# Optimization experiments

Measured on AMD Instinct MI355X. Metric: run time of the kernel, lower is better.

Reference implementation:

```python
import jax, jax.numpy as jnp
import numpy as np

B, K, C, NCLS = 256, 32, 2048, 20
EPS = 1e-4
MARGIN = 150.0
TRIP_MARGIN = 0.8
T = 0.07


def setup_inputs() -> dict:
    key = jax.random.key(0)
    ks = jax.random.split(key, 8)
    video_scores = jax.random.uniform(ks[0], (B, NCLS), jnp.float32, EPS, 1.0 - EPS)
    label = (jax.random.uniform(ks[1], (B, NCLS)) < 0.15).astype(jnp.float32)
    # guarantee every video has at least one positive class (avoids div-by-zero in label norm)
    fix = jax.nn.one_hot(jax.random.randint(ks[2], (B,), 0, NCLS), NCLS, dtype=jnp.float32)
    label = jnp.where((label.sum(axis=1, keepdims=True) > 0), label, fix)
    PA = jax.random.normal(ks[3], (B, K, C), jnp.float32)
    PB = jax.random.normal(ks[4], (B, K, C), jnp.float32)
    NA = jax.random.normal(ks[5], (B, K, C), jnp.float32)
    NB = jax.random.normal(ks[6], (B, K, C), jnp.float32)
    return {"video_scores": video_scores, "label": label, "PA": PA, "PB": PB, "NA": NA, "NB": NB}


def _nce(q, k, neg):
    # q,k: [B,C]; neg: [B,K,C] -> permuted to [B,C,K], normalized over C
    q = q / jnp.linalg.norm(q, axis=1, keepdims=True)
    k = k / jnp.linalg.norm(k, axis=1, keepdims=True)
    negp = jnp.transpose(neg, (0, 2, 1))  # [B,C,K]
    negp = negp / jnp.linalg.norm(negp, axis=1, keepdims=True)
    l_pos = jnp.einsum('nc,nc->n', q, k)[:, None]        # [B,1]
    l_neg = jnp.einsum('nc,nck->nk', q, negp)            # [B,K]
    logits = jnp.concatenate([l_pos, l_neg], axis=1) / T
    # CE with target class 0
    return -jax.nn.log_softmax(logits, axis=1)[:, 0].mean()


def _triplet(label, PA):
    n = label.shape[0]
    act = PA.mean(axis=2)  # [B,K] -- original averages over channels per snippet
    an = act / jnp.linalg.norm(act, axis=1, keepdims=True)
    D = 1.0 - an @ an.T    # [B,B] pairwise cosine distance
    idxs = jnp.arange(n)

    def per_class(m):  # m: bool [B] membership of this class
        cnt = m.sum()
        # anchor = last element of the Python set iteration = max member index
        anchor = jnp.max(jnp.where(m, idxs, -1))
        row = D[anchor]
        others = idxs != anchor
        max_d = jnp.maximum(0.0, jnp.max(jnp.where(m & others, row, -jnp.inf)))
        min_d = jnp.minimum(jnp.max(row), jnp.min(jnp.where(~m, row, jnp.inf)))
        contrib = jnp.maximum(max_d - min_d + TRIP_MARGIN, 0.0)
        return jnp.where(cnt > 1, contrib, 0.0)

    masks = (label == 1).T  # [NCLS, B]
    return jax.vmap(per_class)(masks).sum()


def reference(video_scores, label, PA, PB, NA, NB):
    # Action (BCE) loss with row-normalized labels
    lbl = label / label.sum(axis=1, keepdims=True)
    p = video_scores
    loss_cls = -(lbl * jnp.log(p) + (1.0 - lbl) * jnp.log(1.0 - p)).mean()

    # SniCo NCE
    loss_snico = _nce(NA.mean(axis=1), PA.mean(axis=1), PB) + _nce(NB.mean(axis=1), PB.mean(axis=1), PA)

    # Abs (uncertainty-margin) loss
    la = jnp.maximum(MARGIN - jnp.linalg.norm(PA.mean(axis=1), axis=1), 0.0)
    lb = jnp.linalg.norm(PB.mean(axis=1), axis=1)
    loss_abs = jnp.mean((la + lb) ** 2)

    # Triplet loss (vectorized version of the serial mining)
    loss_triplet = _triplet(label, PA)

    loss_total = loss_cls + 0.01 * loss_snico + 0.0005 * loss_abs + 0.005 * loss_triplet
    return (loss_total, loss_cls, loss_snico, loss_abs, loss_triplet)
```

## Files before the change

### kernel.cpp

```cpp
#include <hip/hip_runtime.h>
#include <math.h>

#define BATCH 256
#define KSNIP 32
#define CH    2048
#define CH4   512
#define NCLSS 20

#define OFF_MNA 0
#define OFF_MNB 524288
#define OFF_PK  1048576
#define PKN 8192
#define OFF_SC  1089536

__device__ __forceinline__ float dot4(float4 a, float4 b) {
    return a.x*b.x + a.y*b.y + a.z*b.z + a.w*b.w;
}
__device__ __forceinline__ float sum4(float4 a) { return a.x + a.y + a.z + a.w; }
__device__ __forceinline__ float4 add4(float4 a, float4 b) {
    return make_float4(a.x+b.x, a.y+b.y, a.z+b.z, a.w+b.w);
}

__global__ __launch_bounds__(512) void meanNK_kernel(
    const float* __restrict__ NAp, const float* __restrict__ NBp,
    float* __restrict__ ws)
{
    const int t   = blockIdx.x >> 8;
    const int b   = blockIdx.x & 255;
    const int tid = threadIdx.x;
    const int w   = tid >> 6;
    const int l   = tid & 63;

    const float4* src = (const float4*)((t ? NBp : NAp) + (size_t)b * KSNIP * CH);

    float4 cs[8];
    #pragma unroll
    for (int j = 0; j < 8; ++j) cs[j] = make_float4(0.f,0.f,0.f,0.f);

    #pragma unroll
    for (int kk = 0; kk < 4; ++kk) {
        const int k = w + kk*8;
        float4 v[8];
        #pragma unroll
        for (int j = 0; j < 8; ++j) v[j] = src[k*CH4 + l + j*64];
        #pragma unroll
        for (int j = 0; j < 8; ++j) cs[j] = add4(cs[j], v[j]);
    }

    __shared__ float4 sCol[CH4];
    __shared__ float  sW[8];
    for (int wv = 0; wv < 8; ++wv) {
        if (w == wv) {
            #pragma unroll
            for (int j = 0; j < 8; ++j) {
                const int c = l + j*64;
                sCol[c] = (wv == 0) ? cs[j] : add4(sCol[c], cs[j]);
            }
        }
        __syncthreads();
    }

    float4 m = sCol[tid];
    const float s = 1.0f/32.0f;
    m.x *= s; m.y *= s; m.z *= s; m.w *= s;
    ((float4*)(ws + (t ? OFF_MNB : OFF_MNA) + b*CH))[tid] = m;

    float v2 = dot4(m, m);
    #pragma unroll
    for (int o = 32; o; o >>= 1) v2 += __shfl_xor(v2, o);
    if (l == 0) sW[w] = v2;
    __syncthreads();
    if (tid == 0) {
        float tot = 0.f;
        #pragma unroll
        for (int i = 0; i < 8; ++i) tot += sW[i];
        ws[OFF_SC + (2 + t)*256 + b] = tot;
    }
}

__global__ __launch_bounds__(512) void dots_kernel(
    const float* __restrict__ PA, const float* __restrict__ PB,
    float* __restrict__ ws)
{
    const int t   = blockIdx.x >> 8;
    const int b   = blockIdx.x & 255;
    const int tid = threadIdx.x;
    const int w   = tid >> 6;
    const int l   = tid & 63;

    const float4* src = (const float4*)((t ? PB : PA) + (size_t)b * KSNIP * CH);

    __shared__ float4 sDot[CH4];
    __shared__ float4 sDap[CH4];
    __shared__ float4 sCol[CH4];
    __shared__ float  sW[8][2];

    sDot[tid] = ((const float4*)(ws + (t ? OFF_MNA : OFF_MNB)))[b*CH4 + tid];
    sDap[tid] = ((const float4*)(ws + (t ? OFF_MNB : OFF_MNA)))[b*CH4 + tid];
    __syncthreads();

    float4 cs[8];
    #pragma unroll
    for (int j = 0; j < 8; ++j) cs[j] = make_float4(0.f,0.f,0.f,0.f);

    #pragma unroll
    for (int kk = 0; kk < 4; ++kk) {
        const int k = w + kk*8;
        float4 v[8];
        #pragma unroll
        for (int j = 0; j < 8; ++j) v[j] = src[k*CH4 + l + j*64];

        float dq = 0.f, sq = 0.f, rs = 0.f;
        #pragma unroll
        for (int j = 0; j < 8; ++j) {
            cs[j] = add4(cs[j], v[j]);
            float4 om = sDot[l + j*64];
            dq += dot4(om, v[j]);
            sq += dot4(v[j], v[j]);
            rs += sum4(v[j]);
        }
        #pragma unroll
        for (int o = 32; o; o >>= 1) {
            dq += __shfl_xor(dq, o);
            sq += __shfl_xor(sq, o);
            rs += __shfl_xor(rs, o);
        }
        if (l == 0) {
            const int idx = k*BATCH + b;
            if (t == 0) {
                ws[OFF_PK + 2*PKN + idx] = dq;
                ws[OFF_PK + 3*PKN + idx] = sq;
                ws[OFF_PK + 4*PKN + idx] = rs;
            } else {
                ws[OFF_PK + 0*PKN + idx] = dq;
                ws[OFF_PK + 1*PKN + idx] = sq;
            }
        }
    }

    for (int wv = 0; wv < 8; ++wv) {
        if (w == wv) {
            #pragma unroll
            for (int j = 0; j < 8; ++j) {
                const int c = l + j*64;
                sCol[c] = (wv == 0) ? cs[j] : add4(sCol[c], cs[j]);
            }
        }
        __syncthreads();
    }

    float4 m = sCol[tid];
    const float s = 1.0f/32.0f;
    m.x *= s; m.y *= s; m.z *= s; m.w *= s;
    float n2  = dot4(m, m);
    float dap = dot4(sDap[tid], m);
    #pragma unroll
    for (int o = 32; o; o >>= 1) {
        n2  += __shfl_xor(n2, o);
        dap += __shfl_xor(dap, o);
    }
    if (l == 0) { sW[w][0] = n2; sW[w][1] = dap; }
    __syncthreads();
    if (tid == 0) {
        float t0 = 0.f, t1 = 0.f;
        #pragma unroll
        for (int i = 0; i < 8; ++i) { t0 += sW[i][0]; t1 += sW[i][1]; }
        ws[OFF_SC + t*256 + b]       = t0;
        ws[OFF_SC + (4 + t)*256 + b] = t1;
    }
}

__global__ __launch_bounds__(256) void finish_kernel(
    const float* __restrict__ vs, const float* __restrict__ label,
    const float* __restrict__ ws, float* __restrict__ out)
{
    const int tid  = threadIdx.x;
    const int b    = tid;
    const int lane = tid & 63;
    const int w    = tid >> 6;

    __shared__ float sLab[NCLSS*BATCH];
    __shared__ float sVS [NCLSS*BATCH];
    __shared__ float an[BATCH][33];
    __shared__ float sD[NCLSS][BATCH];
    __shared__ unsigned long long sMask[NCLSS][4];
    __shared__ int   sAnchor[NCLSS];
    __shared__ int   sCnt[NCLSS];
    __shared__ float sbuf[4];
    __shared__ float stp[4];

    const float* pk = ws + OFF_PK;

    #pragma unroll
    for (int j = 0; j < NCLSS; ++j) {
        const int i = j*BATCH + tid;
        const int c = i % NCLSS;
        const int bb = i / NCLSS;
        sLab[c*BATCH + bb] = label[i];
        sVS [c*BATCH + bb] = vs[i];
    }
    #pragma unroll
    for (int j = 0; j < KSNIP; ++j) {
        const int i = j*BATCH + tid;
        an[i & 255][i >> 8] = pk[4*PKN + i];
    }
    __syncthreads();

    {
        float nrm = 0.f;
        #pragma unroll
        for (int k = 0; k < KSNIP; ++k) { float v = an[b][k]; nrm += v*v; }
        const float inv = 1.0f / sqrtf(nrm);
        #pragma unroll
        for (int k = 0; k < KSNIP; ++k) an[b][k] *= inv;
    }

    const float invT = 1.0f / 0.07f;
    const float nPA = sqrtf(ws[OFF_SC + 0*256 + b]);
    const float nPB = sqrtf(ws[OFF_SC + 1*256 + b]);
    const float nNA = sqrtf(ws[OFF_SC + 2*256 + b]);
    const float nNB = sqrtf(ws[OFF_SC + 3*256 + b]);
    const float dAP = ws[OFF_SC + 4*256 + b];
    const float dBP = ws[OFF_SC + 5*256 + b];

    float nce;
    {
        const float lpos = dAP / (nNA * nPA) * invT;
        float vv[KSNIP];
        #pragma unroll
        for (int k = 0; k < KSNIP; ++k) {
            const float dq = pk[0*PKN + k*BATCH + b];
            const float sq = pk[1*PKN + k*BATCH + b];
            vv[k] = dq * invT / (nNA * sqrtf(sq));
        }
        float m = lpos;
        #pragma unroll
        for (int k = 0; k < KSNIP; ++k) m = fmaxf(m, vv[k]);
        float s = expf(lpos - m);
        #pragma unroll
        for (int k = 0; k < KSNIP; ++k) s += expf(vv[k] - m);
        nce = logf(s) + m - lpos;
    }
    {
        const float lpos = dBP / (nNB * nPB) * invT;
        float vv[KSNIP];
        #pragma unroll
        for (int k = 0; k < KSNIP; ++k) {
            const float dq = pk[2*PKN + k*BATCH + b];
            const float sq = pk[3*PKN + k*BATCH + b];
            vv[k] = dq * invT / (nNB * sqrtf(sq));
        }
        float m = lpos;
        #pragma unroll
        for (int k = 0; k < KSNIP; ++k) m = fmaxf(m, vv[k]);
        float s = expf(lpos - m);
        #pragma unroll
        for (int k = 0; k < KSNIP; ++k) s += expf(vv[k] - m);
        nce += logf(s) + m - lpos;
    }

    const float la   = fmaxf(150.0f - nPA, 0.0f);
    const float absb = (la + nPB) * (la + nPB);

    float rs = 0.0f;
    #pragma unroll
    for (int c = 0; c < NCLSS; ++c) rs += sLab[c*BATCH + b];
    float clsb = 0.0f;
    #pragma unroll
    for (int c = 0; c < NCLSS; ++c) {
        const float l = sLab[c*BATCH + b] / rs;
        const float p = sVS [c*BATCH + b];
        clsb -= l * logf(p) + (1.0f - l) * logf(1.0f - p);
    }

    auto blocksum = [&](float v) -> float {
        #pragma unroll
        for (int o = 32; o; o >>= 1) v += __shfl_xor(v, o);
        __syncthreads();
        if (lane == 0) sbuf[w] = v;
        __syncthreads();
        return sbuf[0] + sbuf[1] + sbuf[2] + sbuf[3];
    };

    const float loss_snico = blocksum(nce)  / 256.0f;
    const float loss_abs   = blocksum(absb) / 256.0f;
    const float loss_cls   = blocksum(clsb) / 5120.0f;

    #pragma unroll
    for (int c = 0; c < NCLSS; ++c) {
        const bool mm = sLab[c*BATCH + b] > 0.5f;
        const unsigned long long mk = __ballot(mm);
        if (lane == 0) sMask[c][w] = mk;
    }
    __syncthreads();
    if (tid < NCLSS) {
        int cnt = 0, anchor = -1;
        #pragma unroll
        for (int q = 3; q >= 0; --q) {
            const unsigned long long mq = sMask[tid][q];
            cnt += __builtin_popcountll(mq);
            if (anchor < 0 && mq) anchor = q*64 + 63 - __builtin_clzll(mq);
        }
        sAnchor[tid] = anchor;
        sCnt[tid]    = cnt;
    }
    __syncthreads();

    #pragma unroll
    for (int c = 0; c < NCLSS; ++c) {
        if (sCnt[c] > 1) {
            const int a = sAnchor[c];
            float acc = 0.f;
            #pragma unroll
            for (int k = 0; k < KSNIP; ++k) acc += an[a][k] * an[b][k];
            sD[c][b] = 1.0f - acc;
        }
    }
    __syncthreads();

    float tripw = 0.f;
    #pragma unroll
    for (int cc = 0; cc < 5; ++cc) {
        const int c = w*5 + cc;
        if (sCnt[c] > 1) {
            const int a = sAnchor[c];
            float vAll = -__builtin_inff();
            float vMem = -__builtin_inff();
            float vNon =  __builtin_inff();
            #pragma unroll
            for (int q = 0; q < 4; ++q) {
                const int bb = lane + q*64;
                const float d = sD[c][bb];
                const bool mm = (sMask[c][q] >> lane) & 1ull;
                vAll = fmaxf(vAll, d);
                if (mm && bb != a) vMem = fmaxf(vMem, d);
                if (!mm)           vNon = fminf(vNon, d);
            }
            #pragma unroll
            for (int o = 32; o; o >>= 1) {
                vAll = fmaxf(vAll, __shfl_xor(vAll, o));
                vMem = fmaxf(vMem, __shfl_xor(vMem, o));
                vNon = fminf(vNon, __shfl_xor(vNon, o));
            }
            if (lane == 0) {
                const float max_d = fmaxf(0.0f, vMem);
                const float min_d = fminf(vAll, vNon);
                tripw += fmaxf(max_d - min_d + 0.8f, 0.0f);
            }
        }
    }
    if (lane == 0) stp[w] = tripw;
    __syncthreads();

    if (tid == 0) {
        const float trip_total = stp[0] + stp[1] + stp[2] + stp[3];
        const float total = loss_cls + 0.01f * loss_snico + 0.0005f * loss_abs + 0.005f * trip_total;
        out[0] = total;
        out[1] = loss_cls;
        out[2] = loss_snico;
        out[3] = loss_abs;
        out[4] = trip_total;
    }
}

extern "C" void kernel_launch(void* const* d_in, const int* in_sizes, int n_in,
                              void* d_out, int out_size, void* d_ws, size_t ws_size,
                              hipStream_t stream) {
    const float* vs    = (const float*)d_in[0];
    const float* label = (const float*)d_in[1];
    const float* PA    = (const float*)d_in[2];
    const float* PB    = (const float*)d_in[3];
    const float* NAp   = (const float*)d_in[4];
    const float* NBp   = (const float*)d_in[5];
    float* ws  = (float*)d_ws;
    float* out = (float*)d_out;

    meanNK_kernel<<<dim3(512), dim3(512), 0, stream>>>(NAp, NBp, ws);
    dots_kernel  <<<dim3(512), dim3(512), 0, stream>>>(PA, PB, ws);
    finish_kernel<<<dim3(1),   dim3(256), 0, stream>>>(vs, label, ws, out);
}
```

Baseline: 85.14 us.

## Split per-batch reductions across four channel-quarter blocks with atomic partial sums

```diff
diff --git a/kernel.cpp b/kernel.cpp
--- a/kernel.cpp
+++ b/kernel.cpp
@@ -11,7 +11,7 @@
 #define OFF_MNB 524288
 #define OFF_PK  1048576
 #define PKN 8192
-#define OFF_SC  1089536
+#define OFF_SC2 1089536
 
 __device__ __forceinline__ float dot4(float4 a, float4 b) {
     return a.x*b.x + a.y*b.y + a.z*b.z + a.w*b.w;
@@ -21,104 +21,106 @@
     return make_float4(a.x+b.x, a.y+b.y, a.z+b.z, a.w+b.w);
 }
 
-__global__ __launch_bounds__(512) void meanNK_kernel(
+__global__ __launch_bounds__(256, 8) void meanNK_kernel(
     const float* __restrict__ NAp, const float* __restrict__ NBp,
     float* __restrict__ ws)
 {
-    const int t   = blockIdx.x >> 8;
-    const int b   = blockIdx.x & 255;
+    const int idx = blockIdx.x;
+    const int t   = idx >> 10;
+    const int b   = (idx >> 2) & 255;
+    const int q   = idx & 3;
     const int tid = threadIdx.x;
     const int w   = tid >> 6;
     const int l   = tid & 63;
+    const int cb  = q*128;
+
+    if (tid < 20) ws[OFF_PK + idx*20 + tid] = 0.0f;
 
     const float4* src = (const float4*)((t ? NBp : NAp) + (size_t)b * KSNIP * CH);
 
-    float4 cs[8];
-    #pragma unroll
-    for (int j = 0; j < 8; ++j) cs[j] = make_float4(0.f,0.f,0.f,0.f);
-
-    #pragma unroll
-    for (int kk = 0; kk < 4; ++kk) {
-        const int k = w + kk*8;
-        float4 v[8];
-        #pragma unroll
-        for (int j = 0; j < 8; ++j) v[j] = src[k*CH4 + l + j*64];
-        #pragma unroll
-        for (int j = 0; j < 8; ++j) cs[j] = add4(cs[j], v[j]);
-    }
-
-    __shared__ float4 sCol[CH4];
-    __shared__ float  sW[8];
-    for (int wv = 0; wv < 8; ++wv) {
-        if (w == wv) {
-            #pragma unroll
-            for (int j = 0; j < 8; ++j) {
-                const int c = l + j*64;
-                sCol[c] = (wv == 0) ? cs[j] : add4(sCol[c], cs[j]);
-            }
+    float4 cs0 = {0,0,0,0}, cs1 = {0,0,0,0};
+    float4 v[2][2];
+    v[0][0] = src[w*CH4 + cb + l];
+    v[0][1] = src[w*CH4 + cb + l + 64];
+
+    #pragma unroll
+    for (int kk = 0; kk < 8; ++kk) {
+        if (kk < 7) {
+            const int k = w + (kk+1)*4;
+            v[(kk+1)&1][0] = src[k*CH4 + cb + l];
+            v[(kk+1)&1][1] = src[k*CH4 + cb + l + 64];
+        }
+        cs0 = add4(cs0, v[kk&1][0]);
+        cs1 = add4(cs1, v[kk&1][1]);
+    }
+
+    __shared__ float4 sCol[128];
+    __shared__ float  sn[4];
+    #pragma unroll
+    for (int p = 0; p < 4; ++p) {
+        if (w == p) {
+            if (p == 0) { sCol[l] = cs0; sCol[l+64] = cs1; }
+            else        { sCol[l] = add4(sCol[l], cs0); sCol[l+64] = add4(sCol[l+64], cs1); }
         }
         __syncthreads();
     }
 
-    float4 m = sCol[tid];
-    const float s = 1.0f/32.0f;
-    m.x *= s; m.y *= s; m.z *= s; m.w *= s;
-    ((float4*)(ws + (t ? OFF_MNB : OFF_MNA) + b*CH))[tid] = m;
-
-    float v2 = dot4(m, m);
-    #pragma unroll
-    for (int o = 32; o; o >>= 1) v2 += __shfl_xor(v2, o);
-    if (l == 0) sW[w] = v2;
-    __syncthreads();
-    if (tid == 0) {
-        float tot = 0.f;
-        #pragma unroll
-        for (int i = 0; i < 8; ++i) tot += sW[i];
-        ws[OFF_SC + (2 + t)*256 + b] = tot;
-    }
-}
-
-__global__ __launch_bounds__(512) void dots_kernel(
+    float n2p = 0.0f;
+    if (tid < 128) {
+        float4 m = sCol[tid];
+        const float s = 1.0f/32.0f;
+        m.x *= s; m.y *= s; m.z *= s; m.w *= s;
+        ((float4*)(ws + (t ? OFF_MNB : OFF_MNA) + b*CH))[cb + tid] = m;
+        n2p = dot4(m, m);
+    }
+    #pragma unroll
+    for (int o = 32; o; o >>= 1) n2p += __shfl_xor(n2p, o);
+    if (l == 0) sn[w] = n2p;
+    __syncthreads();
+    if (tid == 0)
+        ws[OFF_SC2 + (2 + t)*1024 + b*4 + q] = sn[0]+sn[1]+sn[2]+sn[3];
+}
+
+__global__ __launch_bounds__(256, 8) void dots_kernel(
     const float* __restrict__ PA, const float* __restrict__ PB,
     float* __restrict__ ws)
 {
-    const int t   = blockIdx.x >> 8;
-    const int b   = blockIdx.x & 255;
+    const int idx = blockIdx.x;
+    const int t   = idx >> 10;
+    const int b   = (idx >> 2) & 255;
+    const int q   = idx & 3;
     const int tid = threadIdx.x;
     const int w   = tid >> 6;
     const int l   = tid & 63;
-
-    const float4* src = (const float4*)((t ? PB : PA) + (size_t)b * KSNIP * CH);
-
-    __shared__ float4 sDot[CH4];
-    __shared__ float4 sDap[CH4];
-    __shared__ float4 sCol[CH4];
-    __shared__ float  sW[8][2];
-
-    sDot[tid] = ((const float4*)(ws + (t ? OFF_MNA : OFF_MNB)))[b*CH4 + tid];
-    sDap[tid] = ((const float4*)(ws + (t ? OFF_MNB : OFF_MNA)))[b*CH4 + tid];
-    __syncthreads();
-
-    float4 cs[8];
-    #pragma unroll
-    for (int j = 0; j < 8; ++j) cs[j] = make_float4(0.f,0.f,0.f,0.f);
-
-    #pragma unroll
-    for (int kk = 0; kk < 4; ++kk) {
-        const int k = w + kk*8;
-        float4 v[8];
-        #pragma unroll
-        for (int j = 0; j < 8; ++j) v[j] = src[k*CH4 + l + j*64];
-
-        float dq = 0.f, sq = 0.f, rs = 0.f;
-        #pragma unroll
-        for (int j = 0; j < 8; ++j) {
-            cs[j] = add4(cs[j], v[j]);
-            float4 om = sDot[l + j*64];
-            dq += dot4(om, v[j]);
-            sq += dot4(v[j], v[j]);
-            rs += sum4(v[j]);
-        }
+    const int cb  = q*128;
+
+    const float4* src  = (const float4*)((t ? PB : PA) + (size_t)b * KSNIP * CH);
+    const float4* mDot = (const float4*)(ws + (t ? OFF_MNA : OFF_MNB) + b*CH);
+    const float4* mDap = (const float4*)(ws + (t ? OFF_MNB : OFF_MNA) + b*CH);
+    float* pk = ws + OFF_PK;
+
+    const float4 md0 = mDot[cb + l];
+    const float4 md1 = mDot[cb + l + 64];
+
+    float4 cs0 = {0,0,0,0}, cs1 = {0,0,0,0};
+    float4 v[2][2];
+    v[0][0] = src[w*CH4 + cb + l];
+    v[0][1] = src[w*CH4 + cb + l + 64];
+
+    #pragma unroll
+    for (int kk = 0; kk < 8; ++kk) {
+        if (kk < 7) {
+            const int k = w + (kk+1)*4;
+            v[(kk+1)&1][0] = src[k*CH4 + cb + l];
+            v[(kk+1)&1][1] = src[k*CH4 + cb + l + 64];
+        }
+        const float4 a = v[kk&1][0];
+        const float4 c = v[kk&1][1];
+        cs0 = add4(cs0, a);
+        cs1 = add4(cs1, c);
+        float dq = dot4(md0, a) + dot4(md1, c);
+        float sq = dot4(a, a)   + dot4(c, c);
+        float rs = sum4(a)      + sum4(c);
         #pragma unroll
         for (int o = 32; o; o >>= 1) {
             dq += __shfl_xor(dq, o);
@@ -126,47 +128,48 @@
             rs += __shfl_xor(rs, o);
         }
         if (l == 0) {
-            const int idx = k*BATCH + b;
+            const int k   = w + kk*4;
+            const int id2 = k*BATCH + b;
             if (t == 0) {
-                ws[OFF_PK + 2*PKN + idx] = dq;
-                ws[OFF_PK + 3*PKN + idx] = sq;
-                ws[OFF_PK + 4*PKN + idx] = rs;
+                atomicAdd(pk + 2*PKN + id2, dq);
+                atomicAdd(pk + 3*PKN + id2, sq);
+                atomicAdd(pk + 4*PKN + id2, rs);
             } else {
-                ws[OFF_PK + 0*PKN + idx] = dq;
-                ws[OFF_PK + 1*PKN + idx] = sq;
+                atomicAdd(pk + 0*PKN + id2, dq);
+                atomicAdd(pk + 1*PKN + id2, sq);
             }
         }
     }
 
-    for (int wv = 0; wv < 8; ++wv) {
-        if (w == wv) {
-            #pragma unroll
-            for (int j = 0; j < 8; ++j) {
-                const int c = l + j*64;
-                sCol[c] = (wv == 0) ? cs[j] : add4(sCol[c], cs[j]);
-            }
+    __shared__ float4 sCol[128];
+    __shared__ float  sn[4][2];
+    #pragma unroll
+    for (int p = 0; p < 4; ++p) {
+        if (w == p) {
+            if (p == 0) { sCol[l] = cs0; sCol[l+64] = cs1; }
+            else        { sCol[l] = add4(sCol[l], cs0); sCol[l+64] = add4(sCol[l+64], cs1); }
         }
         __syncthreads();
     }
 
-    float4 m = sCol[tid];
-    const float s = 1.0f/32.0f;
-    m.x *= s; m.y *= s; m.z *= s; m.w *= s;
-    float n2  = dot4(m, m);
-    float dap = dot4(sDap[tid], m);
+    float n2p = 0.0f, dapp = 0.0f;
+    if (tid < 128) {
+        float4 m = sCol[tid];
+        const float s = 1.0f/32.0f;
+        m.x *= s; m.y *= s; m.z *= s; m.w *= s;
+        n2p  = dot4(m, m);
+        dapp = dot4(mDap[cb + tid], m);
+    }
     #pragma unroll
     for (int o = 32; o; o >>= 1) {
-        n2  += __shfl_xor(n2, o);
-        dap += __shfl_xor(dap, o);
-    }
-    if (l == 0) { sW[w][0] = n2; sW[w][1] = dap; }
+        n2p  += __shfl_xor(n2p, o);
+        dapp += __shfl_xor(dapp, o);
+    }
+    if (l == 0) { sn[w][0] = n2p; sn[w][1] = dapp; }
     __syncthreads();
     if (tid == 0) {
-        float t0 = 0.f, t1 = 0.f;
-        #pragma unroll
-        for (int i = 0; i < 8; ++i) { t0 += sW[i][0]; t1 += sW[i][1]; }
-        ws[OFF_SC + t*256 + b]       = t0;
-        ws[OFF_SC + (4 + t)*256 + b] = t1;
+        ws[OFF_SC2 + t*1024       + b*4 + q] = sn[0][0]+sn[1][0]+sn[2][0]+sn[3][0];
+        ws[OFF_SC2 + (4 + t)*1024 + b*4 + q] = sn[0][1]+sn[1][1]+sn[2][1]+sn[3][1];
     }
 }
 
@@ -189,7 +192,8 @@
     __shared__ float sbuf[4];
     __shared__ float stp[4];
 
-    const float* pk = ws + OFF_PK;
+    const float* pk  = ws + OFF_PK;
+    const float* sc2 = ws + OFF_SC2;
 
     #pragma unroll
     for (int j = 0; j < NCLSS; ++j) {
@@ -215,13 +219,18 @@
         for (int k = 0; k < KSNIP; ++k) an[b][k] *= inv;
     }
 
+    auto rd4 = [&](int j) -> float {
+        const float* p = sc2 + j*1024 + b*4;
+        return p[0] + p[1] + p[2] + p[3];
+    };
+
     const float invT = 1.0f / 0.07f;
-    const float nPA = sqrtf(ws[OFF_SC + 0*256 + b]);
-    const float nPB = sqrtf(ws[OFF_SC + 1*256 + b]);
-    const float nNA = sqrtf(ws[OFF_SC + 2*256 + b]);
-    const float nNB = sqrtf(ws[OFF_SC + 3*256 + b]);
-    const float dAP = ws[OFF_SC + 4*256 + b];
-    const float dBP = ws[OFF_SC + 5*256 + b];
+    const float nPA = sqrtf(rd4(0));
+    const float nPB = sqrtf(rd4(1));
+    const float nNA = sqrtf(rd4(2));
+    const float nNB = sqrtf(rd4(3));
+    const float dAP = rd4(4);
+    const float dBP = rd4(5);
 
     float nce;
     {
@@ -296,10 +305,10 @@
     if (tid < NCLSS) {
         int cnt = 0, anchor = -1;
         #pragma unroll
-        for (int q = 3; q >= 0; --q) {
-            const unsigned long long mq = sMask[tid][q];
+        for (int qq = 3; qq >= 0; --qq) {
+            const unsigned long long mq = sMask[tid][qq];
             cnt += __builtin_popcountll(mq);
-            if (anchor < 0 && mq) anchor = q*64 + 63 - __builtin_clzll(mq);
+            if (anchor < 0 && mq) anchor = qq*64 + 63 - __builtin_clzll(mq);
         }
         sAnchor[tid] = anchor;
         sCnt[tid]    = cnt;
@@ -328,10 +337,10 @@
             float vMem = -__builtin_inff();
             float vNon =  __builtin_inff();
             #pragma unroll
-            for (int q = 0; q < 4; ++q) {
-                const int bb = lane + q*64;
+            for (int qq = 0; qq < 4; ++qq) {
+                const int bb = lane + qq*64;
                 const float d = sD[c][bb];
-                const bool mm = (sMask[c][q] >> lane) & 1ull;
+                const bool mm = (sMask[c][qq] >> lane) & 1ull;
                 vAll = fmaxf(vAll, d);
                 if (mm && bb != a) vMem = fmaxf(vMem, d);
                 if (!mm)           vNon = fminf(vNon, d);
@@ -375,7 +384,7 @@
     float* ws  = (float*)d_ws;
     float* out = (float*)d_out;
 
-    meanNK_kernel<<<dim3(512), dim3(512), 0, stream>>>(NAp, NBp, ws);
-    dots_kernel  <<<dim3(512), dim3(512), 0, stream>>>(PA, PB, ws);
-    finish_kernel<<<dim3(1),   dim3(256), 0, stream>>>(vs, label, ws, out);
-}
+    meanNK_kernel<<<dim3(2048), dim3(256), 0, stream>>>(NAp, NBp, ws);
+    dots_kernel  <<<dim3(2048), dim3(256), 0, stream>>>(PA, PB, ws);
+    finish_kernel<<<dim3(1),    dim3(256), 0, stream>>>(vs, label, ws, out);
+}
```

Measured after the change: 110.3 us. 1.3x slower.
